# Kernel tuning notes

Hardware: AMD Instinct MI355X
Metric: run time of the kernel (lower is better)

Reference implementation:

```python
import jax, jax.numpy as jnp
import numpy as np

B, CD, NF, V, D = 16384, 13, 26, 100000, 64
BOT = [256, 128]
TOP = [512, 256, 128]
NUM_EMB = NF + 1            # 27 (bottom output + 26 categorical)
NUM_INTER = NUM_EMB * (NUM_EMB - 1) // 2  # 351
TOP_IN = NUM_INTER + NUM_EMB * D          # 2079
BN_INV = 1.0 / np.sqrt(1.0 + 1e-5)        # eval-mode BatchNorm: running_mean=0, running_var=1


def _lin(key, fan_in, fan_out):
    kw, kb = jax.random.split(key)
    s = 1.0 / np.sqrt(fan_in)
    W = jax.random.uniform(kw, (fan_in, fan_out), minval=-s, maxval=s, dtype=jnp.float32)
    b = jax.random.uniform(kb, (fan_out,), minval=-s, maxval=s, dtype=jnp.float32)
    return W, b


def setup_inputs() -> dict:
    key = jax.random.key(0)
    ks = jax.random.split(key, 16)
    continuous = jax.random.normal(ks[0], (B, CD), dtype=jnp.float32)
    cat_idx = jax.random.randint(ks[1], (B, NF), 0, V, dtype=jnp.int32)
    emb_tables = jax.random.normal(ks[2], (NF, V, D), dtype=jnp.float32)  # nn.Embedding init ~ N(0,1)
    W1, b1 = _lin(ks[3], CD, BOT[0]);   g1 = jnp.ones((BOT[0],)); be1 = jnp.zeros((BOT[0],))
    W2, b2 = _lin(ks[4], BOT[0], BOT[1]); g2 = jnp.ones((BOT[1],)); be2 = jnp.zeros((BOT[1],))
    W3, b3 = _lin(ks[5], BOT[1], D)
    W4, b4 = _lin(ks[6], TOP_IN, TOP[0]); g4 = jnp.ones((TOP[0],)); be4 = jnp.zeros((TOP[0],))
    W5, b5 = _lin(ks[7], TOP[0], TOP[1]); g5 = jnp.ones((TOP[1],)); be5 = jnp.zeros((TOP[1],))
    W6, b6 = _lin(ks[8], TOP[1], TOP[2]); g6 = jnp.ones((TOP[2],)); be6 = jnp.zeros((TOP[2],))
    W7, b7 = _lin(ks[9], TOP[2], 1)
    return dict(continuous=continuous, cat_idx=cat_idx, emb_tables=emb_tables,
                W1=W1, b1=b1, g1=g1, be1=be1, W2=W2, b2=b2, g2=g2, be2=be2, W3=W3, b3=b3,
                W4=W4, b4=b4, g4=g4, be4=be4, W5=W5, b5=b5, g5=g5, be5=be5,
                W6=W6, b6=b6, g6=g6, be6=be6, W7=W7, b7=b7)


def _bn(x, g, b):
    # eval-mode BatchNorm1d with running_mean=0, running_var=1
    return g * (x * BN_INV) + b


def reference(continuous, cat_idx, emb_tables,
              W1, b1, g1, be1, W2, b2, g2, be2, W3, b3,
              W4, b4, g4, be4, W5, b5, g5, be5, W6, b6, g6, be6, W7, b7):
    # Bottom MLP: 13 -> 256 -> 128 -> 64
    h = jax.nn.relu(_bn(continuous @ W1 + b1, g1, be1))
    h = jax.nn.relu(_bn(h @ W2 + b2, g2, be2))
    bottom = h @ W3 + b3                         # [B, D]

    # Embedding gather: one table per categorical feature
    emb = emb_tables[jnp.arange(NF), cat_idx]    # [B, NF, D]
    all_emb = jnp.concatenate([bottom[:, None, :], emb], axis=1)  # [B, 27, D]

    # Pairwise dot-product interactions via one bmm + triu gather
    Z = jnp.einsum('bnd,bmd->bnm', all_emb, all_emb)              # [B, 27, 27]
    iu, ju = np.triu_indices(NUM_EMB, k=1)                        # row-major i<j (matches torch loop order)
    inter = Z[:, iu, ju]                                          # [B, 351]

    top_in = jnp.concatenate([inter, all_emb.reshape(all_emb.shape[0], -1)], axis=1)  # [B, 2079]

    # Top MLP: 2079 -> 512 -> 256 -> 128 -> 1
    t = jax.nn.relu(_bn(top_in @ W4 + b4, g4, be4))
    t = jax.nn.relu(_bn(t @ W5 + b5, g5, be5))
    t = jax.nn.relu(_bn(t @ W6 + b6, g6, be6))
    scores = t @ W7 + b7                                          # [B, 1]
    return scores
```

## Files before the change

### kernel.cpp

```cpp
#include <hip/hip_runtime.h>
#include <stdint.h>
#include <stddef.h>

#define BATCH   16384
#define CDIM    13
#define NFEAT   26
#define VROWS   100000
#define EDIM    64
#define NEMB    27
#define NINTER  351
#define TOPIN   2079
#define KP4     2112
#define BN_INVF 0.9999950000374997f

typedef __attribute__((ext_vector_type(8)))  __bf16 bf16x8;
typedef __attribute__((ext_vector_type(4)))  float  f32x4;
typedef __attribute__((ext_vector_type(16))) float  f32x16;
typedef __attribute__((ext_vector_type(4)))  uint32_t uint4v;

__device__ __forceinline__ uint32_t f2bf(float f){
  uint32_t u = __float_as_uint(f);
  return (u + 0x7fffu + ((u >> 16) & 1u)) >> 16;
}
__device__ __forceinline__ float bf2f(uint32_t h){ return __uint_as_float(h << 16); }
__device__ __forceinline__ uint32_t pack2(float a, float b){
  return f2bf(a) | (f2bf(b) << 16);
}
__device__ __forceinline__ void async_load16(const void* g, void* l){
  __builtin_amdgcn_global_load_lds(
      (const __attribute__((address_space(1))) uint32_t*)g,
      (__attribute__((address_space(3))) uint32_t*)l, 16, 0, 0);
}
__device__ __forceinline__ int rswz(int row){ return ((row ^ (row >> 3)) & 7) << 3; }

__device__ __forceinline__ void transpose_tile(
    float (*tile)[65], const float* __restrict__ src, unsigned short* __restrict__ dst,
    int K, int N, int Kpad, int remap, int kb, int nb){
  int k0 = kb*64, n0 = nb*64, t = threadIdx.x;
  int srcBase = remap ? ((k0 < 1728) ? (k0 + 351) : (k0 - 1728)) : k0;
  #pragma unroll 4
  for(int p = 0; p < 16; p++){
    int kr = p*4 + (t >> 6), nc = t & 63;
    float v = 0.f;
    if(k0 + kr < K && (n0 + nc) < N) v = src[(size_t)(srcBase + kr) * N + n0 + nc];
    tile[kr][nc] = v;
  }
  __syncthreads();
  #pragma unroll 4
  for(int p = 0; p < 16; p++){
    int nr = p*4 + (t >> 6), kc = t & 63;
    if(k0 + kc < Kpad && (n0 + nr) < N)
      dst[(size_t)(n0 + nr) * Kpad + k0 + kc] = (unsigned short)f2bf(tile[kc][nr]);
  }
}

__global__ __launch_bounds__(256) void prep(
    const float* __restrict__ cont,
    const float* __restrict__ W1, const float* __restrict__ W2, const float* __restrict__ W3,
    const float* __restrict__ W4, const float* __restrict__ W5, const float* __restrict__ W6,
    unsigned short* __restrict__ xphi, unsigned short* __restrict__ xplo,
    unsigned short* __restrict__ W1t, unsigned short* __restrict__ W2t,
    unsigned short* __restrict__ W3t, unsigned short* __restrict__ W4t,
    unsigned short* __restrict__ W5t, unsigned short* __restrict__ W6t){
  __shared__ float tile[64][65];
  int bid = blockIdx.x;
  if(bid < 264){ transpose_tile(tile, W4, W4t, TOPIN, 512, KP4, 1, bid % 33, bid / 33); }
  else if(bid < 296){ int r = bid-264; transpose_tile(tile, W5, W5t, 512, 256, 512, 0, r % 8, r / 8); }
  else if(bid < 304){ int r = bid-296; transpose_tile(tile, W6, W6t, 256, 128, 256, 0, r % 4, r / 4); }
  else if(bid < 312){ int r = bid-304; transpose_tile(tile, W2, W2t, 256, 128, 256, 0, r % 4, r / 4); }
  else if(bid < 314){ int r = bid-312; transpose_tile(tile, W3, W3t, 128, 64, 128, 0, r, 0); }
  else if(bid < 318){ int r = bid-314; transpose_tile(tile, W1, W1t, CDIM, 256, 32, 0, 0, r); }
  else {
    int row = (bid - 318) * 256 + threadIdx.x;
    const float* xr = cont + (size_t)row * CDIM;
    uint32_t uh[16], ul[16];
    #pragma unroll
    for(int k = 0; k < 16; k++){
      uint32_t h0=0, h1=0, l0=0, l1=0;
      if(2*k < CDIM){
        float x = xr[2*k]; h0 = f2bf(x); l0 = f2bf(x - bf2f(h0));
      }
      if(2*k+1 < CDIM){
        float x = xr[2*k+1]; h1 = f2bf(x); l1 = f2bf(x - bf2f(h1));
      }
      uh[k] = h0 | (h1 << 16);
      ul[k] = l0 | (l1 << 16);
    }
    #pragma unroll
    for(int s = 0; s < 4; s++){
      uint4v vh, vl;
      #pragma unroll
      for(int e = 0; e < 4; e++){ vh[e] = uh[4*s+e]; vl[e] = ul[4*s+e]; }
      *(uint4v*)(xphi + (size_t)row*32 + s*8) = vh;
      *(uint4v*)(xplo + (size_t)row*32 + s*8) = vl;
    }
  }
}

__global__ __launch_bounds__(256) void bottom_mfma(
    const unsigned short* __restrict__ xphi, const unsigned short* __restrict__ xplo,
    const unsigned short* __restrict__ W1t, const unsigned short* __restrict__ W2t,
    const unsigned short* __restrict__ W3t,
    const float* __restrict__ b1, const float* __restrict__ g1, const float* __restrict__ be1,
    const float* __restrict__ b2, const float* __restrict__ g2, const float* __restrict__ be2,
    const float* __restrict__ b3,
    unsigned short* __restrict__ bottomBF){
  __shared__ unsigned short h1hi[64*256];
  __shared__ unsigned short h1lo[64*256];
  __shared__ unsigned short h2hi[64*128];
  __shared__ unsigned short h2lo[64*128];
  int t = threadIdx.x, w = t >> 6, l = t & 63;
  int m0 = blockIdx.x * 64;
  int lr = l & 15, lk = (l >> 4) * 8;

  {
    bf16x8 axh[4], axl[4];
    #pragma unroll
    for(int mt = 0; mt < 4; mt++){
      size_t ro = (size_t)(m0 + mt*16 + lr) * 32 + lk;
      axh[mt] = *(const bf16x8*)(xphi + ro);
      axl[mt] = *(const bf16x8*)(xplo + ro);
    }
    #pragma unroll
    for(int nt = 0; nt < 4; nt++){
      int n = (w*4 + nt)*16 + lr;
      bf16x8 bw = *(const bf16x8*)(W1t + (size_t)n*32 + lk);
      f32x4 acc[4];
      #pragma unroll
      for(int mt = 0; mt < 4; mt++){
        #pragma unroll
        for(int e = 0; e < 4; e++) acc[mt][e] = 0.f;
        acc[mt] = __builtin_amdgcn_mfma_f32_16x16x32_bf16(axh[mt], bw, acc[mt], 0, 0, 0);
        acc[mt] = __builtin_amdgcn_mfma_f32_16x16x32_bf16(axl[mt], bw, acc[mt], 0, 0, 0);
      }
      float sc = g1[n]*BN_INVF, bo = be1[n], bi = b1[n];
      #pragma unroll
      for(int mt = 0; mt < 4; mt++){
        #pragma unroll
        for(int q = 0; q < 4; q++){
          int row = mt*16 + (l >> 4)*4 + q;
          float y = fmaxf(sc*(acc[mt][q] + bi) + bo, 0.f);
          uint32_t hb = f2bf(y);
          int idx = row*256 + (n ^ rswz(row));
          h1hi[idx] = (unsigned short)hb;
          h1lo[idx] = (unsigned short)f2bf(y - bf2f(hb));
        }
      }
    }
  }
  __syncthreads();

  {
    f32x4 acc[4][2];
    #pragma unroll
    for(int mt = 0; mt < 4; mt++)
      #pragma unroll
      for(int nt = 0; nt < 2; nt++)
        #pragma unroll
        for(int e = 0; e < 4; e++) acc[mt][nt][e] = 0.f;
    for(int ks = 0; ks < 8; ks++){
      bf16x8 bw[2];
      #pragma unroll
      for(int nt = 0; nt < 2; nt++){
        int n = (w*2 + nt)*16 + lr;
        bw[nt] = *(const bf16x8*)(W2t + (size_t)n*256 + ks*32 + lk);
      }
      #pragma unroll
      for(int mt = 0; mt < 4; mt++){
        int row = mt*16 + lr;
        int idx = row*256 + ((ks*32 + lk) ^ rswz(row));
        bf16x8 ah = *(const bf16x8*)(h1hi + idx);
        bf16x8 al = *(const bf16x8*)(h1lo + idx);
        #pragma unroll
        for(int nt = 0; nt < 2; nt++){
          acc[mt][nt] = __builtin_amdgcn_mfma_f32_16x16x32_bf16(ah, bw[nt], acc[mt][nt], 0, 0, 0);
          acc[mt][nt] = __builtin_amdgcn_mfma_f32_16x16x32_bf16(al, bw[nt], acc[mt][nt], 0, 0, 0);
        }
      }
    }
    #pragma unroll
    for(int nt = 0; nt < 2; nt++){
      int n = (w*2 + nt)*16 + lr;
      float sc = g2[n]*BN_INVF, bo = be2[n], bi = b2[n];
      #pragma unroll
      for(int mt = 0; mt < 4; mt++){
        #pragma unroll
        for(int q = 0; q < 4; q++){
          int row = mt*16 + (l >> 4)*4 + q;
          float y = fmaxf(sc*(acc[mt][nt][q] + bi) + bo, 0.f);
          uint32_t hb = f2bf(y);
          int idx = row*128 + (n ^ rswz(row));
          h2hi[idx] = (unsigned short)hb;
          h2lo[idx] = (unsigned short)f2bf(y - bf2f(hb));
        }
      }
    }
  }
  __syncthreads();

  {
    f32x4 acc[4];
    #pragma unroll
    for(int mt = 0; mt < 4; mt++)
      #pragma unroll
      for(int e = 0; e < 4; e++) acc[mt][e] = 0.f;
    int n = w*16 + lr;
    for(int ks = 0; ks < 4; ks++){
      bf16x8 bw = *(const bf16x8*)(W3t + (size_t)n*128 + ks*32 + lk);
      #pragma unroll
      for(int mt = 0; mt < 4; mt++){
        int row = mt*16 + lr;
        int idx = row*128 + ((ks*32 + lk) ^ rswz(row));
        bf16x8 ah = *(const bf16x8*)(h2hi + idx);
        bf16x8 al = *(const bf16x8*)(h2lo + idx);
        acc[mt] = __builtin_amdgcn_mfma_f32_16x16x32_bf16(ah, bw, acc[mt], 0, 0, 0);
        acc[mt] = __builtin_amdgcn_mfma_f32_16x16x32_bf16(al, bw, acc[mt], 0, 0, 0);
      }
    }
    float bi = b3[n];
    #pragma unroll
    for(int mt = 0; mt < 4; mt++){
      #pragma unroll
      for(int q = 0; q < 4; q++){
        int row = m0 + mt*16 + (l >> 4)*4 + q;
        bottomBF[(size_t)row*64 + n] = (unsigned short)f2bf(acc[mt][q] + bi);
      }
    }
  }
}

__global__ __launch_bounds__(256) void interact(
    const unsigned short* __restrict__ bottomBF, const int* __restrict__ cat_idx,
    const float* __restrict__ emb, unsigned short* __restrict__ top_in){
  __shared__ unsigned short inter_s[4][352];
  int w = threadIdx.x >> 6, l = threadIdx.x & 63;
  int b = blockIdx.x * 4 + w;
  int r = l & 31, h = l >> 5;
  bool active = (r < NEMB);
  uint4v q[4];
  if(active && r == 0){
    const unsigned short* sb = bottomBF + (size_t)b * 64;
    #pragma unroll
    for(int s = 0; s < 4; s++) q[s] = *(const uint4v*)(sb + h*8 + s*16);
  } else if(active){
    int f = r - 1;
    int idx = cat_idx[b * NFEAT + f];
    const float* src = emb + ((size_t)f * VROWS + (size_t)idx) * 64;
    #pragma unroll
    for(int s = 0; s < 4; s++){
      int k0 = h*8 + s*16;
      float4 v0 = *(const float4*)(src + k0);
      float4 v1 = *(const float4*)(src + k0 + 4);
      q[s][0] = pack2(v0.x, v0.y); q[s][1] = pack2(v0.z, v0.w);
      q[s][2] = pack2(v1.x, v1.y); q[s][3] = pack2(v1.z, v1.w);
    }
  } else {
    #pragma unroll
    for(int s = 0; s < 4; s++){ q[s][0]=0; q[s][1]=0; q[s][2]=0; q[s][3]=0; }
  }
  if(active){
    #pragma unroll
    for(int s = 0; s < 4; s++)
      *(uint4v*)(top_in + (size_t)b*KP4 + r*64 + h*8 + s*16) = q[s];
  }
  f32x16 acc;
  #pragma unroll
  for(int i = 0; i < 16; i++) acc[i] = 0.f;
  #pragma unroll
  for(int s = 0; s < 4; s++){
    bf16x8 a = __builtin_bit_cast(bf16x8, q[s]);
    acc = __builtin_amdgcn_mfma_f32_32x32x16_bf16(a, a, acc, 0, 0, 0);
  }
  if(active){
    #pragma unroll
    for(int qq = 0; qq < 16; qq++){
      int i = (qq & 3) + 8*(qq >> 2) + 4*h;
      if(i < r){
        int p = i*(53 - i)/2 + (r - i - 1);
        inter_s[w][p] = (unsigned short)f2bf(acc[qq]);
      }
    }
  }
  __syncthreads();
  size_t basei = (size_t)b*KP4 + 1728;
  for(int t0 = l; t0 < 176; t0 += 64){
    uint32_t lo = inter_s[w][2*t0];
    uint32_t hi = (2*t0 + 1 < NINTER) ? (uint32_t)inter_s[w][2*t0 + 1] : 0u;
    *(uint32_t*)(top_in + basei + 2*t0) = lo | (hi << 16);
  }
  if(l < 16) *(uint32_t*)(top_in + (size_t)b*KP4 + 2080 + 2*l) = 0;
}

template<int KSTEPS, int NB>
__global__ __launch_bounds__(512, 2) void gemm_deep(
    const unsigned short* __restrict__ A, int sA,
    const unsigned short* __restrict__ Bw, int sB,
    const float* __restrict__ bias, const float* __restrict__ gg,
    const float* __restrict__ be,
    unsigned short* __restrict__ out, int sOut){
  __shared__ char smem[3*49152];
  int nwg = gridDim.x;
  int bid = blockIdx.x;
  int lin = (bid & 7) * (nwg >> 3) + (bid >> 3);
  int m0 = (lin / NB) * 256, n0 = (lin % NB) * 128;
  int t = threadIdx.x, w = t >> 6, l = t & 63;
  int wr = (w >> 1) * 64, wc = (w & 1) * 64;
  f32x4 acc[4][4];
  #pragma unroll
  for(int i = 0; i < 4; i++)
    #pragma unroll
    for(int j = 0; j < 4; j++)
      #pragma unroll
      for(int e = 0; e < 4; e++) acc[i][j][e] = 0.f;

  const unsigned short* g[6];
  int ldsOff[6];
  #pragma unroll
  for(int i = 0; i < 6; i++){
    if(i < 4){
      int o = i*8192 + t*16;
      int row = o >> 7;
      int cb  = (o & 127) ^ ((row & 7) << 4);
      g[i] = A + (size_t)(m0 + row)*sA + (cb >> 1);
      ldsOff[i] = o;
    } else {
      int o = (i-4)*8192 + t*16;
      int row = o >> 7;
      int cb  = (o & 127) ^ ((row & 7) << 4);
      g[i] = Bw + (size_t)(n0 + row)*sB + (cb >> 1);
      ldsOff[i] = 32768 + o;
    }
  }
  int lr = l & 15;
  int o1 = ((l >> 4) * 16) ^ ((l & 7) << 4);

  #pragma unroll
  for(int i = 0; i < 6; i++) async_load16(g[i], smem + ldsOff[i]);
  #pragma unroll
  for(int i = 0; i < 6; i++) async_load16(g[i] + 64, smem + 49152 + ldsOff[i]);
  asm volatile("s_waitcnt vmcnt(6)" ::: "memory");
  __builtin_amdgcn_s_barrier();

  for(int kt = 0; kt < KSTEPS; kt++){
    int cur = kt % 3;
    int nxt2 = (kt + 2) % 3;
    int ksrc = (kt + 2 < KSTEPS) ? (kt + 2) : (KSTEPS - 1);
    #pragma unroll
    for(int i = 0; i < 6; i++)
      async_load16(g[i] + ksrc*64, smem + nxt2*49152 + ldsOff[i]);
    const char* bA = smem + cur*49152;
    const char* bB = bA + 32768;
    __builtin_amdgcn_s_setprio(1);
    #pragma unroll
    for(int ks = 0; ks < 2; ks++){
      int ko = o1 ^ (ks << 6);
      bf16x8 af[4], bfr[4];
      #pragma unroll
      for(int x = 0; x < 4; x++){
        af[x]  = *(const bf16x8*)(bA + (wr + x*16 + lr)*128 + ko);
        bfr[x] = *(const bf16x8*)(bB + (wc + x*16 + lr)*128 + ko);
      }
      #pragma unroll
      for(int tr = 0; tr < 4; tr++)
        #pragma unroll
        for(int tc = 0; tc < 4; tc++)
          acc[tr][tc] = __builtin_amdgcn_mfma_f32_16x16x32_bf16(af[tr], bfr[tc], acc[tr][tc], 0, 0, 0);
    }
    __builtin_amdgcn_s_setprio(0);
    asm volatile("s_waitcnt vmcnt(6)" ::: "memory");
    __builtin_amdgcn_s_barrier();
  }

  #pragma unroll
  for(int tc = 0; tc < 4; tc++){
    int n = n0 + wc + tc*16 + lr;
    float sc = gg[n]*BN_INVF, bo = be[n], bi = bias[n];
    #pragma unroll
    for(int tr = 0; tr < 4; tr++){
      int mb = m0 + wr + tr*16 + (l >> 4)*4;
      #pragma unroll
      for(int qq = 0; qq < 4; qq++){
        float y = fmaxf(sc*(acc[tr][tc][qq] + bi) + bo, 0.f);
        out[(size_t)(mb + qq)*sOut + n] = (unsigned short)f2bf(y);
      }
    }
  }
}

template<int KSTEPS, int NB, bool FUSE>
__global__ __launch_bounds__(256) void gemm_top(
    const unsigned short* __restrict__ A, int sA,
    const unsigned short* __restrict__ Bw, int sB,
    const float* __restrict__ bias, const float* __restrict__ gg,
    const float* __restrict__ be,
    unsigned short* __restrict__ out, int sOut,
    const float* __restrict__ W7, const float* __restrict__ b7,
    float* __restrict__ scores){
  __shared__ unsigned short As[128*64];
  __shared__ unsigned short Bs[128*64];
  __shared__ float h6s[FUSE ? 128*132 : 1];
  __shared__ float w7s[FUSE ? 128 : 1];
  int nwg = gridDim.x;
  int bid = blockIdx.x;
  int lin = (bid & 7) * (nwg >> 3) + (bid >> 3);
  int m0 = (lin / NB) * 128, n0 = (lin % NB) * 128;
  int t = threadIdx.x, w = t >> 6, l = t & 63;
  int wr = (w >> 1) * 64, wc = (w & 1) * 64;
  f32x4 acc[4][4];
  #pragma unroll
  for(int i = 0; i < 4; i++)
    #pragma unroll
    for(int j = 0; j < 4; j++)
      #pragma unroll
      for(int e = 0; e < 4; e++) acc[i][j][e] = 0.f;

  const unsigned short* gA[4];
  const unsigned short* gB[4];
  char* ldsA[4];
  char* ldsB[4];
  #pragma unroll
  for(int i = 0; i < 4; i++){
    int o   = w*4096 + i*1024 + l*16;
    int row = o >> 7;
    int cb  = (o & 127) ^ ((row & 7) << 4);
    gA[i] = A  + (size_t)(m0 + row)*sA + (cb >> 1);
    gB[i] = Bw + (size_t)(n0 + row)*sB + (cb >> 1);
    ldsA[i] = (char*)As + o;
    ldsB[i] = (char*)Bs + o;
  }
  int lr = l & 15;
  int o1 = ((l >> 4) * 16) ^ ((l & 7) << 4);

  for(int kt = 0; kt < KSTEPS; kt++){
    #pragma unroll
    for(int i = 0; i < 4; i++){
      async_load16(gA[i] + kt*64, ldsA[i]);
      async_load16(gB[i] + kt*64, ldsB[i]);
    }
    __syncthreads();
    #pragma unroll
    for(int ks = 0; ks < 2; ks++){
      int ko = o1 ^ (ks << 6);
      bf16x8 af[4], bfr[4];
      #pragma unroll
      for(int x = 0; x < 4; x++){
        af[x]  = *(const bf16x8*)((const char*)As + (wr + x*16 + lr)*128 + ko);
        bfr[x] = *(const bf16x8*)((const char*)Bs + (wc + x*16 + lr)*128 + ko);
      }
      #pragma unroll
      for(int tr = 0; tr < 4; tr++)
        #pragma unroll
        for(int tc = 0; tc < 4; tc++)
          acc[tr][tc] = __builtin_amdgcn_mfma_f32_16x16x32_bf16(af[tr], bfr[tc], acc[tr][tc], 0, 0, 0);
    }
    __syncthreads();
  }

  if constexpr(!FUSE){
    #pragma unroll
    for(int tc = 0; tc < 4; tc++){
      int n = n0 + wc + tc*16 + lr;
      float sc = gg[n]*BN_INVF, bo = be[n], bi = bias[n];
      #pragma unroll
      for(int tr = 0; tr < 4; tr++){
        int mb = m0 + wr + tr*16 + (l >> 4)*4;
        #pragma unroll
        for(int qq = 0; qq < 4; qq++){
          float y = fmaxf(sc*(acc[tr][tc][qq] + bi) + bo, 0.f);
          out[(size_t)(mb + qq)*sOut + n] = (unsigned short)f2bf(y);
        }
      }
    }
  } else {
    if(t < 128) w7s[t] = W7[t];
    #pragma unroll
    for(int tc = 0; tc < 4; tc++){
      int n = wc + tc*16 + lr;
      float sc = gg[n0+n]*BN_INVF, bo = be[n0+n], bi = bias[n0+n];
      #pragma unroll
      for(int tr = 0; tr < 4; tr++){
        int mb = wr + tr*16 + (l >> 4)*4;
        #pragma unroll
        for(int qq = 0; qq < 4; qq++)
          h6s[(mb + qq)*132 + n] = fmaxf(sc*(acc[tr][tc][qq] + bi) + bo, 0.f);
      }
    }
    __syncthreads();
    if(t < 128){
      float a7 = b7[0];
      #pragma unroll 8
      for(int c = 0; c < 128; c++) a7 = fmaf(h6s[t*132 + c], w7s[c], a7);
      scores[m0 + t] = a7;
    }
  }
}

static inline size_t alignup(size_t x){ return (x + 255) & ~(size_t)255; }

extern "C" void kernel_launch(void* const* d_in, const int* in_sizes, int n_in,
                              void* d_out, int out_size, void* d_ws, size_t ws_size,
                              hipStream_t stream){
  const float* cont = (const float*)d_in[0];
  const int*   cat  = (const int*)  d_in[1];
  const float* emb  = (const float*)d_in[2];
  const float* W1 = (const float*)d_in[3],  *b1 = (const float*)d_in[4];
  const float* g1 = (const float*)d_in[5],  *be1= (const float*)d_in[6];
  const float* W2 = (const float*)d_in[7],  *b2 = (const float*)d_in[8];
  const float* g2 = (const float*)d_in[9],  *be2= (const float*)d_in[10];
  const float* W3 = (const float*)d_in[11], *b3 = (const float*)d_in[12];
  const float* W4 = (const float*)d_in[13], *b4 = (const float*)d_in[14];
  const float* g4 = (const float*)d_in[15], *be4= (const float*)d_in[16];
  const float* W5 = (const float*)d_in[17], *b5 = (const float*)d_in[18];
  const float* g5 = (const float*)d_in[19], *be5= (const float*)d_in[20];
  const float* W6 = (const float*)d_in[21], *b6 = (const float*)d_in[22];
  const float* g6 = (const float*)d_in[23], *be6= (const float*)d_in[24];
  const float* W7 = (const float*)d_in[25], *b7 = (const float*)d_in[26];

  char* ws = (char*)d_ws;
  unsigned short* bottomBF = (unsigned short*)ws; ws += alignup((size_t)BATCH*64*2);
  unsigned short* xphi = (unsigned short*)ws; ws += alignup((size_t)BATCH*32*2);
  unsigned short* xplo = (unsigned short*)ws; ws += alignup((size_t)BATCH*32*2);
  unsigned short* W1t  = (unsigned short*)ws; ws += alignup((size_t)256*32*2);
  unsigned short* W2t  = (unsigned short*)ws; ws += alignup((size_t)128*256*2);
  unsigned short* W3t  = (unsigned short*)ws; ws += alignup((size_t)64*128*2);
  unsigned short* topi = (unsigned short*)ws; ws += alignup((size_t)BATCH*KP4*2);
  unsigned short* W4t  = (unsigned short*)ws; ws += alignup((size_t)512*KP4*2);
  unsigned short* W5t  = (unsigned short*)ws; ws += alignup((size_t)256*512*2);
  unsigned short* W6t  = (unsigned short*)ws; ws += alignup((size_t)128*256*2);
  unsigned short* h4   = (unsigned short*)ws; ws += alignup((size_t)BATCH*512*2);
  unsigned short* h5   = (unsigned short*)ws; ws += alignup((size_t)BATCH*256*2);
  (void)ws_size; (void)n_in; (void)in_sizes; (void)out_size;

  hipLaunchKernelGGL(prep, dim3(382), dim3(256), 0, stream,
                     cont, W1, W2, W3, W4, W5, W6,
                     xphi, xplo, W1t, W2t, W3t, W4t, W5t, W6t);
  hipLaunchKernelGGL(bottom_mfma, dim3(BATCH/64), dim3(256), 0, stream,
                     xphi, xplo, W1t, W2t, W3t,
                     b1, g1, be1, b2, g2, be2, b3, bottomBF);
  hipLaunchKernelGGL(interact, dim3(BATCH/4), dim3(256), 0, stream, bottomBF, cat, emb, topi);
  hipLaunchKernelGGL((gemm_deep<33, 4>), dim3(256), dim3(512), 0, stream,
                     topi, KP4, W4t, KP4, b4, g4, be4, h4, 512);
  hipLaunchKernelGGL((gemm_top<8, 2, false>), dim3(256), dim3(256), 0, stream,
                     h4, 512, W5t, 512, b5, g5, be5, h5, 256,
                     (const float*)nullptr, (const float*)nullptr, (float*)nullptr);
  hipLaunchKernelGGL((gemm_top<4, 1, true>), dim3(128), dim3(256), 0, stream,
                     h5, 256, W6t, 256, b6, g6, be6, (unsigned short*)nullptr, 0,
                     W7, b7, (float*)d_out);
}
```

Measured before the change: 119.3 us.

## Fuse layers 5-7 into one kernel and split deep GEMM k-step loads

Replaces the two gemm_top launches (layer 5 writing h5 to global, then layer 6+7) with a single gemm_tail kernel. It computes a 64-row tile of h5 into LDS, streams W6 in two halves, and reduces the final 128->1 dot with shuffles. This removes the h5 global round trip and one launch. It also restructures the gemm_deep main loop to issue prefetch loads in two halves interleaved with the two k-substeps, adding extra barriers. Each tail block reloads all of W5 per 64 rows, and only 256 blocks run for the tail.

```diff
diff --git a/kernel.cpp b/kernel.cpp
--- a/kernel.cpp
+++ b/kernel.cpp
@@ -345,153 +345,232 @@
     int cur = kt % 3;
     int nxt2 = (kt + 2) % 3;
     int ksrc = (kt + 2 < KSTEPS) ? (kt + 2) : (KSTEPS - 1);
-    #pragma unroll
-    for(int i = 0; i < 6; i++)
-      async_load16(g[i] + ksrc*64, smem + nxt2*49152 + ldsOff[i]);
     const char* bA = smem + cur*49152;
     const char* bB = bA + 32768;
-    __builtin_amdgcn_s_setprio(1);
+    #pragma unroll
+    for(int i = 0; i < 3; i++)
+      async_load16(g[i] + ksrc*64, smem + nxt2*49152 + ldsOff[i]);
+    {
+      bf16x8 af[4], bfr[4];
+      #pragma unroll
+      for(int x = 0; x < 4; x++){
+        af[x]  = *(const bf16x8*)(bA + (wr + x*16 + lr)*128 + o1);
+        bfr[x] = *(const bf16x8*)(bB + (wc + x*16 + lr)*128 + o1);
+      }
+      __builtin_amdgcn_s_barrier();
+      __builtin_amdgcn_s_setprio(1);
+      #pragma unroll
+      for(int tr = 0; tr < 4; tr++)
+        #pragma unroll
+        for(int tc = 0; tc < 4; tc++)
+          acc[tr][tc] = __builtin_amdgcn_mfma_f32_16x16x32_bf16(af[tr], bfr[tc], acc[tr][tc], 0, 0, 0);
+      __builtin_amdgcn_s_setprio(0);
+    }
+    __builtin_amdgcn_s_barrier();
+    #pragma unroll
+    for(int i = 3; i < 6; i++)
+      async_load16(g[i] + ksrc*64, smem + nxt2*49152 + ldsOff[i]);
+    {
+      bf16x8 af[4], bfr[4];
+      int ko = o1 ^ 64;
+      #pragma unroll
+      for(int x = 0; x < 4; x++){
+        af[x]  = *(const bf16x8*)(bA + (wr + x*16 + lr)*128 + ko);
+        bfr[x] = *(const bf16x8*)(bB + (wc + x*16 + lr)*128 + ko);
+      }
+      asm volatile("s_waitcnt vmcnt(6)" ::: "memory");
+      __builtin_amdgcn_s_barrier();
+      __builtin_amdgcn_s_setprio(1);
+      #pragma unroll
+      for(int tr = 0; tr < 4; tr++)
+        #pragma unroll
+        for(int tc = 0; tc < 4; tc++)
+          acc[tr][tc] = __builtin_amdgcn_mfma_f32_16x16x32_bf16(af[tr], bfr[tc], acc[tr][tc], 0, 0, 0);
+      __builtin_amdgcn_s_setprio(0);
+    }
+    __builtin_amdgcn_s_barrier();
+  }
+
+  #pragma unroll
+  for(int tc = 0; tc < 4; tc++){
+    int n = n0 + wc + tc*16 + lr;
+    float sc = gg[n]*BN_INVF, bo = be[n], bi = bias[n];
+    #pragma unroll
+    for(int tr = 0; tr < 4; tr++){
+      int mb = m0 + wr + tr*16 + (l >> 4)*4;
+      #pragma unroll
+      for(int qq = 0; qq < 4; qq++){
+        float y = fmaxf(sc*(acc[tr][tc][qq] + bi) + bo, 0.f);
+        out[(size_t)(mb + qq)*sOut + n] = (unsigned short)f2bf(y);
+      }
+    }
+  }
+}
+
+__global__ __launch_bounds__(256) void gemm_tail(
+    const unsigned short* __restrict__ h4,
+    const unsigned short* __restrict__ W5t,
+    const float* __restrict__ b5, const float* __restrict__ g5, const float* __restrict__ be5,
+    const unsigned short* __restrict__ W6t,
+    const float* __restrict__ b6, const float* __restrict__ g6, const float* __restrict__ be6,
+    const float* __restrict__ W7, const float* __restrict__ b7,
+    float* __restrict__ scores){
+  __shared__ char smem[74752];
+  unsigned short* h5 = (unsigned short*)(smem + 40960);
+  float* pscore = (float*)(smem + 73728);
+  int t = threadIdx.x, w = t >> 6, l = t & 63;
+  int m0 = blockIdx.x * 64;
+  int lr = l & 15;
+  int o1 = ((l >> 4) * 16) ^ ((l & 7) << 4);
+
+  f32x4 acc5[4][4];
+  #pragma unroll
+  for(int i = 0; i < 4; i++)
+    #pragma unroll
+    for(int j = 0; j < 4; j++)
+      #pragma unroll
+      for(int e = 0; e < 4; e++) acc5[i][j][e] = 0.f;
+
+  const unsigned short* gA[2]; int ldsA[2];
+  #pragma unroll
+  for(int i = 0; i < 2; i++){
+    int o = i*4096 + t*16;
+    int row = o >> 7;
+    int cb = (o & 127) ^ ((row & 7) << 4);
+    gA[i] = h4 + (size_t)(m0 + row)*512 + (cb >> 1);
+    ldsA[i] = o;
+  }
+  const unsigned short* gB[8]; int ldsB[8];
+  #pragma unroll
+  for(int i = 0; i < 8; i++){
+    int o = i*4096 + t*16;
+    int row = o >> 7;
+    int cb = (o & 127) ^ ((row & 7) << 4);
+    gB[i] = W5t + (size_t)row*512 + (cb >> 1);
+    ldsB[i] = 8192 + o;
+  }
+
+  for(int kt = 0; kt < 8; kt++){
+    #pragma unroll
+    for(int i = 0; i < 2; i++) async_load16(gA[i] + kt*64, smem + ldsA[i]);
+    #pragma unroll
+    for(int i = 0; i < 8; i++) async_load16(gB[i] + kt*64, smem + ldsB[i]);
+    __syncthreads();
     #pragma unroll
     for(int ks = 0; ks < 2; ks++){
       int ko = o1 ^ (ks << 6);
       bf16x8 af[4], bfr[4];
       #pragma unroll
       for(int x = 0; x < 4; x++){
-        af[x]  = *(const bf16x8*)(bA + (wr + x*16 + lr)*128 + ko);
-        bfr[x] = *(const bf16x8*)(bB + (wc + x*16 + lr)*128 + ko);
+        af[x]  = *(const bf16x8*)(smem + (x*16 + lr)*128 + ko);
+        bfr[x] = *(const bf16x8*)(smem + 8192 + (w*64 + x*16 + lr)*128 + ko);
       }
       #pragma unroll
       for(int tr = 0; tr < 4; tr++)
         #pragma unroll
         for(int tc = 0; tc < 4; tc++)
-          acc[tr][tc] = __builtin_amdgcn_mfma_f32_16x16x32_bf16(af[tr], bfr[tc], acc[tr][tc], 0, 0, 0);
-    }
-    __builtin_amdgcn_s_setprio(0);
-    asm volatile("s_waitcnt vmcnt(6)" ::: "memory");
-    __builtin_amdgcn_s_barrier();
-  }
-
+          acc5[tr][tc] = __builtin_amdgcn_mfma_f32_16x16x32_bf16(af[tr], bfr[tc], acc5[tr][tc], 0, 0, 0);
+    }
+    __syncthreads();
+  }
+
+  #pragma unroll
+  for(int i = 0; i < 8; i++){
+    int o = i*4096 + t*16;
+    int row = o >> 8;
+    int cb = (o & 255) ^ ((row & 15) << 4);
+    async_load16(W6t + (size_t)row*256 + (cb >> 1), smem + o);
+  }
   #pragma unroll
   for(int tc = 0; tc < 4; tc++){
-    int n = n0 + wc + tc*16 + lr;
-    float sc = gg[n]*BN_INVF, bo = be[n], bi = bias[n];
+    int c = w*64 + tc*16 + lr;
+    float sc = g5[c]*BN_INVF, bo = be5[c], bi = b5[c];
     #pragma unroll
     for(int tr = 0; tr < 4; tr++){
-      int mb = m0 + wr + tr*16 + (l >> 4)*4;
       #pragma unroll
       for(int qq = 0; qq < 4; qq++){
-        float y = fmaxf(sc*(acc[tr][tc][qq] + bi) + bo, 0.f);
-        out[(size_t)(mb + qq)*sOut + n] = (unsigned short)f2bf(y);
-      }
-    }
-  }
-}
-
-template<int KSTEPS, int NB, bool FUSE>
-__global__ __launch_bounds__(256) void gemm_top(
-    const unsigned short* __restrict__ A, int sA,
-    const unsigned short* __restrict__ Bw, int sB,
-    const float* __restrict__ bias, const float* __restrict__ gg,
-    const float* __restrict__ be,
-    unsigned short* __restrict__ out, int sOut,
-    const float* __restrict__ W7, const float* __restrict__ b7,
-    float* __restrict__ scores){
-  __shared__ unsigned short As[128*64];
-  __shared__ unsigned short Bs[128*64];
-  __shared__ float h6s[FUSE ? 128*132 : 1];
-  __shared__ float w7s[FUSE ? 128 : 1];
-  int nwg = gridDim.x;
-  int bid = blockIdx.x;
-  int lin = (bid & 7) * (nwg >> 3) + (bid >> 3);
-  int m0 = (lin / NB) * 128, n0 = (lin % NB) * 128;
-  int t = threadIdx.x, w = t >> 6, l = t & 63;
-  int wr = (w >> 1) * 64, wc = (w & 1) * 64;
-  f32x4 acc[4][4];
+        int row = tr*16 + (l >> 4)*4 + qq;
+        float y = fmaxf(sc*(acc5[tr][tc][qq] + bi) + bo, 0.f);
+        h5[row*256 + (c ^ rswz(row))] = (unsigned short)f2bf(y);
+      }
+    }
+  }
+  __syncthreads();
+
+  f32x4 acc6[4][2];
   #pragma unroll
   for(int i = 0; i < 4; i++)
     #pragma unroll
-    for(int j = 0; j < 4; j++)
-      #pragma unroll
-      for(int e = 0; e < 4; e++) acc[i][j][e] = 0.f;
-
-  const unsigned short* gA[4];
-  const unsigned short* gB[4];
-  char* ldsA[4];
-  char* ldsB[4];
-  #pragma unroll
-  for(int i = 0; i < 4; i++){
-    int o   = w*4096 + i*1024 + l*16;
-    int row = o >> 7;
-    int cb  = (o & 127) ^ ((row & 7) << 4);
-    gA[i] = A  + (size_t)(m0 + row)*sA + (cb >> 1);
-    gB[i] = Bw + (size_t)(n0 + row)*sB + (cb >> 1);
-    ldsA[i] = (char*)As + o;
-    ldsB[i] = (char*)Bs + o;
-  }
-  int lr = l & 15;
-  int o1 = ((l >> 4) * 16) ^ ((l & 7) << 4);
-
-  for(int kt = 0; kt < KSTEPS; kt++){
-    #pragma unroll
-    for(int i = 0; i < 4; i++){
-      async_load16(gA[i] + kt*64, ldsA[i]);
-      async_load16(gB[i] + kt*64, ldsB[i]);
-    }
-    __syncthreads();
-    #pragma unroll
-    for(int ks = 0; ks < 2; ks++){
-      int ko = o1 ^ (ks << 6);
-      bf16x8 af[4], bfr[4];
-      #pragma unroll
-      for(int x = 0; x < 4; x++){
-        af[x]  = *(const bf16x8*)((const char*)As + (wr + x*16 + lr)*128 + ko);
-        bfr[x] = *(const bf16x8*)((const char*)Bs + (wc + x*16 + lr)*128 + ko);
-      }
-      #pragma unroll
-      for(int tr = 0; tr < 4; tr++)
-        #pragma unroll
-        for(int tc = 0; tc < 4; tc++)
-          acc[tr][tc] = __builtin_amdgcn_mfma_f32_16x16x32_bf16(af[tr], bfr[tc], acc[tr][tc], 0, 0, 0);
-    }
-    __syncthreads();
-  }
-
-  if constexpr(!FUSE){
-    #pragma unroll
-    for(int tc = 0; tc < 4; tc++){
-      int n = n0 + wc + tc*16 + lr;
-      float sc = gg[n]*BN_INVF, bo = be[n], bi = bias[n];
-      #pragma unroll
-      for(int tr = 0; tr < 4; tr++){
-        int mb = m0 + wr + tr*16 + (l >> 4)*4;
-        #pragma unroll
-        for(int qq = 0; qq < 4; qq++){
-          float y = fmaxf(sc*(acc[tr][tc][qq] + bi) + bo, 0.f);
-          out[(size_t)(mb + qq)*sOut + n] = (unsigned short)f2bf(y);
-        }
-      }
-    }
-  } else {
-    if(t < 128) w7s[t] = W7[t];
-    #pragma unroll
-    for(int tc = 0; tc < 4; tc++){
-      int n = wc + tc*16 + lr;
-      float sc = gg[n0+n]*BN_INVF, bo = be[n0+n], bi = bias[n0+n];
-      #pragma unroll
-      for(int tr = 0; tr < 4; tr++){
-        int mb = wr + tr*16 + (l >> 4)*4;
-        #pragma unroll
-        for(int qq = 0; qq < 4; qq++)
-          h6s[(mb + qq)*132 + n] = fmaxf(sc*(acc[tr][tc][qq] + bi) + bo, 0.f);
-      }
-    }
-    __syncthreads();
-    if(t < 128){
-      float a7 = b7[0];
-      #pragma unroll 8
-      for(int c = 0; c < 128; c++) a7 = fmaf(h6s[t*132 + c], w7s[c], a7);
-      scores[m0 + t] = a7;
-    }
+    for(int j = 0; j < 2; j++)
+      #pragma unroll
+      for(int e = 0; e < 4; e++) acc6[i][j][e] = 0.f;
+  int lk = (l >> 4) * 8;
+  int lk2 = (l >> 4) * 16;
+  #pragma unroll
+  for(int half = 0; half < 2; half++){
+    if(half == 1){
+      __syncthreads();
+      #pragma unroll
+      for(int i = 0; i < 8; i++){
+        int o = i*4096 + t*16;
+        int row = o >> 8;
+        int cb = (o & 255) ^ ((row & 15) << 4);
+        async_load16(W6t + (size_t)row*256 + 128 + (cb >> 1), smem + o);
+      }
+      __syncthreads();
+    }
+    #pragma unroll
+    for(int ks = 0; ks < 4; ks++){
+      bf16x8 af6[4], bfr6[2];
+      #pragma unroll
+      for(int mt = 0; mt < 4; mt++){
+        int row = mt*16 + lr;
+        af6[mt] = *(const bf16x8*)(h5 + row*256 + ((half*128 + ks*32 + lk) ^ rswz(row)));
+      }
+      #pragma unroll
+      for(int nt = 0; nt < 2; nt++){
+        int row = w*32 + nt*16 + lr;
+        bfr6[nt] = *(const bf16x8*)(smem + row*256 + ((ks*64 + lk2) ^ (lr << 4)));
+      }
+      #pragma unroll
+      for(int mt = 0; mt < 4; mt++)
+        #pragma unroll
+        for(int nt = 0; nt < 2; nt++)
+          acc6[mt][nt] = __builtin_amdgcn_mfma_f32_16x16x32_bf16(af6[mt], bfr6[nt], acc6[mt][nt], 0, 0, 0);
+    }
+  }
+
+  float pr[16];
+  #pragma unroll
+  for(int nt = 0; nt < 2; nt++){
+    int c = w*32 + nt*16 + lr;
+    float sc = g6[c]*BN_INVF, bo = be6[c], bi = b6[c];
+    float w7c = W7[c];
+    #pragma unroll
+    for(int mt = 0; mt < 4; mt++){
+      #pragma unroll
+      for(int qq = 0; qq < 4; qq++){
+        float v = fmaxf(sc*(acc6[mt][nt][qq] + bi) + bo, 0.f) * w7c;
+        if(nt == 0) pr[mt*4 + qq] = v; else pr[mt*4 + qq] += v;
+      }
+    }
+  }
+  #pragma unroll
+  for(int mask = 1; mask < 16; mask <<= 1){
+    #pragma unroll
+    for(int i = 0; i < 16; i++) pr[i] += __shfl_xor(pr[i], mask, 64);
+  }
+  if(lr == 0){
+    #pragma unroll
+    for(int mt = 0; mt < 4; mt++)
+      #pragma unroll
+      for(int qq = 0; qq < 4; qq++)
+        pscore[w*64 + mt*16 + (l >> 4)*4 + qq] = pr[mt*4 + qq];
+  }
+  __syncthreads();
+  if(t < 64){
+    float s = b7[0] + pscore[t] + pscore[64 + t] + pscore[128 + t] + pscore[192 + t];
+    scores[m0 + t] = s;
   }
 }
 
@@ -528,7 +607,6 @@
   unsigned short* W5t  = (unsigned short*)ws; ws += alignup((size_t)256*512*2);
   unsigned short* W6t  = (unsigned short*)ws; ws += alignup((size_t)128*256*2);
   unsigned short* h4   = (unsigned short*)ws; ws += alignup((size_t)BATCH*512*2);
-  unsigned short* h5   = (unsigned short*)ws; ws += alignup((size_t)BATCH*256*2);
   (void)ws_size; (void)n_in; (void)in_sizes; (void)out_size;
 
   hipLaunchKernelGGL(prep, dim3(382), dim3(256), 0, stream,
@@ -540,10 +618,6 @@
   hipLaunchKernelGGL(interact, dim3(BATCH/4), dim3(256), 0, stream, bottomBF, cat, emb, topi);
   hipLaunchKernelGGL((gemm_deep<33, 4>), dim3(256), dim3(512), 0, stream,
                      topi, KP4, W4t, KP4, b4, g4, be4, h4, 512);
-  hipLaunchKernelGGL((gemm_top<8, 2, false>), dim3(256), dim3(256), 0, stream,
-                     h4, 512, W5t, 512, b5, g5, be5, h5, 256,
-                     (const float*)nullptr, (const float*)nullptr, (float*)nullptr);
-  hipLaunchKernelGGL((gemm_top<4, 1, true>), dim3(128), dim3(256), 0, stream,
-                     h5, 256, W6t, 256, b6, g6, be6, (unsigned short*)nullptr, 0,
-                     W7, b7, (float*)d_out);
-}
+  hipLaunchKernelGGL(gemm_tail, dim3(256), dim3(256), 0, stream,
+                     h4, W5t, b5, g5, be5, W6t, b6, g6, be6, W7, b7, (float*)d_out);
+}
```

Result: faster. 115.9 us (-2.8%).
